# Optimization experiments

Measured on AMD Instinct MI355X. Metric: run time of the kernel, lower is better.

## Reference

```python
import jax, jax.numpy as jnp
import numpy as np
from jax import lax

B, C, IC, H, W = 4, 64, 32, 64, 64


def _conv(x, w, b, stride, pad):
    y = lax.conv_general_dilated(
        x, w, (stride, stride), [(pad, pad), (pad, pad)],
        dimension_numbers=('NCHW', 'OIHW', 'NCHW'))
    return y + b[None, :, None, None]


def setup_inputs() -> dict:
    key = jax.random.key(0)
    ks = jax.random.split(key, 15)
    s = 0.05
    inp = {
        'x': jax.random.normal(ks[0], (B, C, H, W), jnp.float32),
        # GEunit convs (3x3)
        'd1_w': jax.random.normal(ks[1], (C, C, 3, 3), jnp.float32) * s,
        'd1_b': jax.random.normal(ks[2], (C,), jnp.float32) * s,
        'd2_w': jax.random.normal(ks[3], (C, C, 3, 3), jnp.float32) * s,
        'd2_b': jax.random.normal(ks[4], (C,), jnp.float32) * s,
        'd3_w': jax.random.normal(ks[5], (C, C, 3, 3), jnp.float32) * s,
        'd3_b': jax.random.normal(ks[6], (C,), jnp.float32) * s,
        # 1x1 projections
        'g_w': jax.random.normal(ks[7], (IC, C, 1, 1), jnp.float32) * s,
        'g_b': jax.random.normal(ks[8], (IC,), jnp.float32) * s,
        'th_w': jax.random.normal(ks[9], (IC, C, 1, 1), jnp.float32) * s,
        'th_b': jax.random.normal(ks[10], (IC,), jnp.float32) * s,
        'ph_w': jax.random.normal(ks[11], (IC, C, 1, 1), jnp.float32) * s,
        'ph_b': jax.random.normal(ks[12], (IC,), jnp.float32) * s,
        # output projection (zero-init in original; random here for nontrivial baseline)
        'w_w': jax.random.normal(ks[13], (C, IC, 1, 1), jnp.float32) * s,
        'w_b': jax.random.normal(ks[14], (C,), jnp.float32) * s,
    }
    return inp


def _forward(x, d1_w, d1_b, d2_w, d2_b, d3_w, d3_b,
             g_w, g_b, th_w, th_b, ph_w, ph_b, w_w, w_b):
    lrelu = lambda v: jnp.where(v >= 0, v, 0.2 * v)
    y = lrelu(_conv(x, d1_w, d1_b, 2, 1))
    y = lrelu(_conv(y, d2_w, d2_b, 2, 1))
    y = _conv(y, d3_w, d3_b, 2, 1)
    y = jax.image.resize(y, (x.shape[0], x.shape[1], x.shape[2], x.shape[3]),
                         method='bilinear')  # align_corners=False equivalent
    am = jax.nn.sigmoid(y) * x  # attention_map, [B,C,H,W]

    b, c, h, w = am.shape
    n = h * w
    g_x = _conv(am, g_w, g_b, 1, 0).reshape(b, IC, n)      # [B,IC,N]
    theta = _conv(am, th_w, th_b, 1, 0).reshape(b, IC, n)  # [B,IC,N]
    phi = _conv(am, ph_w, ph_b, 1, 0).reshape(b, IC, n)    # [B,IC,N]

    # f[b,i,j] = theta[:, i] . phi[:, j];  softmax over dim=1 (the i axis)
    f = jnp.einsum('bci,bcj->bij', theta, phi)             # [B,N,N]
    f_div_C = jax.nn.softmax(f, axis=1)
    y2 = jnp.einsum('bij,bjc->bic', f_div_C, g_x.transpose(0, 2, 1))  # [B,N,IC]
    y2 = y2.transpose(0, 2, 1).reshape(b, IC, h, w)

    W_y = _conv(y2, w_w, w_b, 1, 0)
    z = W_y + am
    return z * x


def reference(x, d1_w, d1_b, d2_w, d2_b, d3_w, d3_b,
              g_w, g_b, th_w, th_b, ph_w, ph_b, w_w, w_b):
    return _forward(x, d1_w, d1_b, d2_w, d2_b, d3_w, d3_b,
                    g_w, g_b, th_w, th_b, ph_w, ph_b, w_w, w_b)
```

## Files before the change

### kernel.cpp

```cpp
#include <hip/hip_runtime.h>

#define B_ 4
#define C_ 64
#define IC_ 32
#define N_ 4096
#define LOG2E 1.44269504088896341f

typedef __attribute__((ext_vector_type(8))) short short8;
typedef __attribute__((ext_vector_type(4))) float floatx4;
typedef unsigned short ushort_t;

__device__ __forceinline__ unsigned short f2bf(float f) {
  unsigned u = __float_as_uint(f);
  u += 0x7FFFu + ((u >> 16) & 1u);
  return (unsigned short)(u >> 16);
}
__device__ __forceinline__ float bf2f(unsigned short h) {
  return __uint_as_float(((unsigned)h) << 16);
}

__global__ void __launch_bounds__(256) pack_xw_k(
    const float* __restrict__ x, unsigned short* __restrict__ xclp,
    const float* __restrict__ d1_w, const float* __restrict__ d2_w, const float* __restrict__ d3_w,
    const float* __restrict__ th_w, const float* __restrict__ ph_w, const float* __restrict__ g_w,
    const float* __restrict__ th_b, const float* __restrict__ ph_b, const float* __restrict__ g_b,
    unsigned short* __restrict__ wpk, unsigned short* __restrict__ wproj, float* __restrict__ bproj)
{
  __shared__ float s[64][65];
  const int t = threadIdx.x;
  if (blockIdx.x < 256) {
    const int b = blockIdx.x >> 6, h = blockIdx.x & 63;
    for (int idx = t; idx < 4096; idx += 256) {
      int c = idx >> 6, w = idx & 63;
      s[c][w] = x[((size_t)(b * 64 + c)) * 4096 + h * 64 + w];
    }
    __syncthreads();
    for (int idx = t; idx < 4096; idx += 256) {
      int w = idx >> 6, c = idx & 63;
      xclp[(((size_t)b * 66 + h + 1) * 66 + (w + 1)) * 64 + c] = f2bf(s[c][w]);
    }
  } else {
    const int tid = (blockIdx.x - 256) * 256 + t;
    for (int idx = tid; idx < 3 * 36864; idx += 16 * 256) {
      int cv = idx / 36864, r = idx % 36864;
      int tap = r / 4096, r2 = r % 4096;
      int oc = r2 >> 6, ic = r2 & 63;
      const float* src = (cv == 0) ? d1_w : (cv == 1) ? d2_w : d3_w;
      wpk[(size_t)cv * 36864 + tap * 4096 + oc * 64 + ic] = f2bf(src[oc * 576 + ic * 9 + tap]);
    }
    for (int idx = tid; idx < 6144; idx += 16 * 256) {
      int m = idx >> 6, ic = idx & 63;
      float v = (m < 32) ? LOG2E * th_w[m * 64 + ic]
              : (m < 64) ? ph_w[(m - 32) * 64 + ic]
                         : g_w[(m - 64) * 64 + ic];
      wproj[m * 64 + ic] = f2bf(v);
    }
    for (int m = tid; m < 96; m += 16 * 256) {
      bproj[m] = (m < 32) ? LOG2E * th_b[m] : (m < 64) ? ph_b[m - 32] : g_b[m - 64];
    }
  }
}

template<int IN_PW, int OUT_H, bool LRELU, bool OUT_BF16>
__global__ void __launch_bounds__(64) convmf_k(
    const unsigned short* __restrict__ xin, const unsigned short* __restrict__ wp,
    const float* __restrict__ bias, unsigned short* __restrict__ obf,
    float* __restrict__ of32)
{
  constexpr int NTILES = OUT_H * OUT_H / 16;
  const int lane = threadIdx.x;
  const int n15 = lane & 15, quad = lane >> 4;
  int bx = blockIdx.x;
  const int octile = bx & 3; bx >>= 2;
  const int otile = bx % NTILES;
  const int b = bx / NTILES;
  const int o = otile * 16 + n15;
  const int oh = o / OUT_H, ow = o % OUT_H;
  const unsigned short* xb = xin + (size_t)b * IN_PW * IN_PW * 64;
  floatx4 acc = {0.f, 0.f, 0.f, 0.f};
#pragma unroll
  for (int tap = 0; tap < 9; ++tap) {
    const int kh = tap / 3, kw = tap % 3;
    const unsigned short* xpix = xb + ((size_t)(oh * 2 + kh) * IN_PW + (ow * 2 + kw)) * 64;
#pragma unroll
    for (int ks = 0; ks < 2; ++ks) {
      short8 af = *reinterpret_cast<const short8*>(
          wp + ((size_t)tap * 64 + octile * 16 + n15) * 64 + ks * 32 + quad * 8);
      short8 bf = *reinterpret_cast<const short8*>(xpix + ks * 32 + quad * 8);
      acc = __builtin_amdgcn_mfma_f32_16x16x32_bf16(af, bf, acc, 0, 0, 0);
    }
  }
  const float4 bv = *reinterpret_cast<const float4*>(bias + octile * 16 + quad * 4);
  float v[4] = {acc[0] + bv.x, acc[1] + bv.y, acc[2] + bv.z, acc[3] + bv.w};
  if (LRELU) {
#pragma unroll
    for (int r = 0; r < 4; ++r) v[r] = (v[r] >= 0.f) ? v[r] : 0.2f * v[r];
  }
  if (OUT_BF16) {
    constexpr int OPW = OUT_H + 2;
    unsigned short pk[4];
#pragma unroll
    for (int r = 0; r < 4; ++r) pk[r] = f2bf(v[r]);
    *reinterpret_cast<uint2*>(
        obf + (((size_t)b * OPW + oh + 1) * OPW + (ow + 1)) * 64 + octile * 16 + quad * 4) =
        *reinterpret_cast<uint2*>(pk);
  } else {
    *reinterpret_cast<float4*>(
        of32 + ((size_t)b * OUT_H * OUT_H + o) * 64 + octile * 16 + quad * 4) =
        *reinterpret_cast<float4*>(v);
  }
}

__global__ void __launch_bounds__(256) upsproj_k(
    const unsigned short* __restrict__ y2clp, const unsigned short* __restrict__ wp3,
    const float* __restrict__ b3, const float* __restrict__ x,
    const unsigned short* __restrict__ wproj, const float* __restrict__ bproj,
    unsigned short* __restrict__ am_cl, unsigned short* __restrict__ thph,
    unsigned short* __restrict__ g16)
{
  const int b = blockIdx.x >> 6, oh = blockIdx.x & 63;
  const int t = threadIdx.x;
  __shared__ float s0[512], s1[512];
  __shared__ unsigned short s_am[64][72];
  float sh = (oh + 0.5f) * 0.125f - 0.5f;
  float fh = floorf(sh); float ah = sh - fh; int h0 = (int)fh;
  int h0c = min(7, max(0, h0)), h1c = min(7, max(0, h0 + 1));
  {
    const int wave = t >> 6, lane = t & 63;
    const int n15 = lane & 15, quad = lane >> 4;
    const int hrow = (n15 < 8) ? h0c : h1c;
    const int ow8 = n15 & 7;
    const unsigned short* xb2 = y2clp + (size_t)b * 18 * 18 * 64;
    floatx4 acc = {0.f, 0.f, 0.f, 0.f};
#pragma unroll
    for (int tap = 0; tap < 9; ++tap) {
      const int kh = tap / 3, kw = tap % 3;
      const unsigned short* xpix = xb2 + ((size_t)(hrow * 2 + kh) * 18 + (ow8 * 2 + kw)) * 64;
#pragma unroll
      for (int ks = 0; ks < 2; ++ks) {
        short8 af = *reinterpret_cast<const short8*>(
            wp3 + ((size_t)tap * 64 + wave * 16 + n15) * 64 + ks * 32 + quad * 8);
        short8 bf = *reinterpret_cast<const short8*>(xpix + ks * 32 + quad * 8);
        acc = __builtin_amdgcn_mfma_f32_16x16x32_bf16(af, bf, acc, 0, 0, 0);
      }
    }
    const float4 bv = *reinterpret_cast<const float4*>(b3 + wave * 16 + quad * 4);
    float4 st = {acc[0] + bv.x, acc[1] + bv.y, acc[2] + bv.z, acc[3] + bv.w};
    float* dst = (n15 < 8) ? s0 : s1;
    *reinterpret_cast<float4*>(&dst[(size_t)ow8 * 64 + wave * 16 + quad * 4]) = st;
  }
  __syncthreads();
  {
    const int ow = t >> 2, cq = t & 3;
    float sw = (ow + 0.5f) * 0.125f - 0.5f;
    float fw = floorf(sw); float aw = sw - fw; int w0 = (int)fw;
    int w0c = min(7, max(0, w0)), w1c = min(7, max(0, w0 + 1));
    const int n = oh * 64 + ow;
    const float* xb = x + (size_t)b * 64 * 4096 + n;
    unsigned short* ap = am_cl + ((size_t)b * N_ + n) * 64 + cq * 16;
#pragma unroll
    for (int u = 0; u < 4; ++u) {
      int c0 = cq * 16 + u * 4;
      float4 a00 = *reinterpret_cast<const float4*>(&s0[w0c * 64 + c0]);
      float4 a01 = *reinterpret_cast<const float4*>(&s0[w1c * 64 + c0]);
      float4 a10 = *reinterpret_cast<const float4*>(&s1[w0c * 64 + c0]);
      float4 a11 = *reinterpret_cast<const float4*>(&s1[w1c * 64 + c0]);
      float i0[4] = {a00.x * (1.f - aw) + a01.x * aw, a00.y * (1.f - aw) + a01.y * aw,
                     a00.z * (1.f - aw) + a01.z * aw, a00.w * (1.f - aw) + a01.w * aw};
      float i1[4] = {a10.x * (1.f - aw) + a11.x * aw, a10.y * (1.f - aw) + a11.y * aw,
                     a10.z * (1.f - aw) + a11.z * aw, a10.w * (1.f - aw) + a11.w * aw};
      unsigned short pk[4];
#pragma unroll
      for (int vi = 0; vi < 4; ++vi) {
        float vv = i0[vi] * (1.f - ah) + i1[vi] * ah;
        float xv = xb[(size_t)(c0 + vi) * 4096];
        float sig = 1.f / (1.f + __expf(-vv));
        pk[vi] = f2bf(sig * xv);
      }
      uint2 pkt = *reinterpret_cast<uint2*>(pk);
      *reinterpret_cast<uint2*>(ap + u * 4) = pkt;
      *reinterpret_cast<uint2*>(&s_am[ow][c0]) = pkt;
    }
  }
  __syncthreads();
  const int wave = t >> 6, lane = t & 63;
  const int n15 = lane & 15, quad = lane >> 4;
  const int n = oh * 64 + wave * 16 + n15;
  const unsigned short* srow = &s_am[wave * 16 + n15][0];
  const short8 bf0 = *reinterpret_cast<const short8*>(srow + quad * 8);
  const short8 bf1 = *reinterpret_cast<const short8*>(srow + 32 + quad * 8);
#pragma unroll
  for (int mt = 0; mt < 6; ++mt) {
    short8 a0 = *reinterpret_cast<const short8*>(wproj + ((size_t)mt * 16 + n15) * 64 + quad * 8);
    short8 a1 = *reinterpret_cast<const short8*>(wproj + ((size_t)mt * 16 + n15) * 64 + 32 + quad * 8);
    floatx4 acc = {0.f, 0.f, 0.f, 0.f};
    acc = __builtin_amdgcn_mfma_f32_16x16x32_bf16(a0, bf0, acc, 0, 0, 0);
    acc = __builtin_amdgcn_mfma_f32_16x16x32_bf16(a1, bf1, acc, 0, 0, 0);
    const float4 bv = *reinterpret_cast<const float4*>(bproj + mt * 16 + quad * 4);
    float v[4] = {acc[0] + bv.x, acc[1] + bv.y, acc[2] + bv.z, acc[3] + bv.w};
    if (mt < 4) {
      unsigned short pk[4];
#pragma unroll
      for (int r = 0; r < 4; ++r) pk[r] = f2bf(v[r]);
      *reinterpret_cast<uint2*>(thph + ((size_t)b * N_ + n) * 64 + mt * 16 + quad * 4) =
          *reinterpret_cast<uint2*>(pk);
    } else {
#pragma unroll
      for (int r = 0; r < 4; ++r)
        g16[((size_t)b * 32 + (mt - 4) * 16 + quad * 4 + r) * N_ + n] = f2bf(v[r]);
    }
  }
}

__global__ void __launch_bounds__(256) attn_stats_k(
    const unsigned short* __restrict__ thph, float* __restrict__ lpart)
{
  const int b  = blockIdx.y;
  const int iz = blockIdx.z;
  const int t = threadIdx.x, wave = t >> 6, lane = t & 63;
  const int n15 = lane & 15, quad = lane >> 4;
  const int jw = blockIdx.x * 256 + wave * 64;
  const unsigned short* base = thph + (size_t)b * N_ * 64;
  short8 bv[4];
#pragma unroll
  for (int v = 0; v < 4; ++v)
    bv[v] = *reinterpret_cast<const short8*>(base + (size_t)(jw + v * 16 + n15) * 64 + 32 + quad * 8);
  float ls[4] = {0.f, 0.f, 0.f, 0.f};
  const unsigned short* ap = base + (size_t)(iz * 256 + n15) * 64 + quad * 8;
  short8 ac = *reinterpret_cast<const short8*>(ap);
  for (int st = 0; st < 16; ++st) {
    short8 an = *reinterpret_cast<const short8*>(ap + (size_t)((st < 15) ? st + 1 : st) * 1024);
#pragma unroll
    for (int v = 0; v < 4; ++v) {
      floatx4 z = {0.f, 0.f, 0.f, 0.f};
      z = __builtin_amdgcn_mfma_f32_16x16x32_bf16(ac, bv[v], z, 0, 0, 0);
      ls[v] += (__builtin_amdgcn_exp2f(z[0]) + __builtin_amdgcn_exp2f(z[1]))
             + (__builtin_amdgcn_exp2f(z[2]) + __builtin_amdgcn_exp2f(z[3]));
    }
    ac = an;
  }
#pragma unroll
  for (int v = 0; v < 4; ++v) {
    ls[v] += __shfl_xor(ls[v], 16);
    ls[v] += __shfl_xor(ls[v], 32);
  }
  if (quad == 0) {
#pragma unroll
    for (int v = 0; v < 4; ++v)
      lpart[((size_t)iz * B_ + b) * N_ + jw + v * 16 + n15] = ls[v];
  }
}

__global__ void __launch_bounds__(256) scale_g_k(
    const float* __restrict__ lpart, unsigned short* __restrict__ g16)
{
  const int b = blockIdx.y;
  const int c0 = blockIdx.z * 8;
  const int j = blockIdx.x * 256 + threadIdx.x;
  float l = 0.f;
#pragma unroll
  for (int iz = 0; iz < 16; ++iz) l += lpart[((size_t)iz * B_ + b) * N_ + j];
  const float rl = 1.f / l;
  unsigned short* gp = g16 + ((size_t)b * 32 + c0) * N_ + j;
#pragma unroll
  for (int c = 0; c < 8; ++c) {
    gp[(size_t)c * N_] = f2bf(bf2f(gp[(size_t)c * N_]) * rl);
  }
}

#define PHI_PITCH 40
#define G_PITCH   136
__global__ void __launch_bounds__(256, 2) attn_pv_k(
    const unsigned short* __restrict__ thph, const unsigned short* __restrict__ g16,
    unsigned short* __restrict__ y2p)
{
  const int b  = blockIdx.y;
  const int jq = blockIdx.z;
  const int t = threadIdx.x, wave = t >> 6, lane = t & 63;
  const int n15 = lane & 15, quad = lane >> 4;
  const int iw = blockIdx.x * 128 + wave * 32;
  const unsigned short* base = thph + (size_t)b * N_ * 64;
  const unsigned short* gs   = g16  + (size_t)b * 32 * N_;
  __shared__ unsigned short phi_lds[2][128 * PHI_PITCH];
  __shared__ unsigned short g_lds[2][32 * G_PITCH];

  const short8 bth0 = *reinterpret_cast<const short8*>(base + (size_t)(iw + n15) * 64 + quad * 8);
  const short8 bth1 = *reinterpret_cast<const short8*>(base + (size_t)(iw + 16 + n15) * 64 + quad * 8);
  floatx4 Y00 = {0.f, 0.f, 0.f, 0.f}, Y01 = {0.f, 0.f, 0.f, 0.f};
  floatx4 Y10 = {0.f, 0.f, 0.f, 0.f}, Y11 = {0.f, 0.f, 0.f, 0.f};

  const int rphi = wave * 32 + (lane >> 2), cph = lane & 3;
  const int cg   = wave * 8  + (lane >> 4), chg = lane & 15;

  uint4 sp0, sp1, sg0, sg1;
  const int jbase = jq * 1024;
  sp0 = *reinterpret_cast<const uint4*>(base + (size_t)(jbase + rphi) * 64 + 32 + cph * 8);
  sp1 = *reinterpret_cast<const uint4*>(base + (size_t)(jbase + rphi + 16) * 64 + 32 + cph * 8);
  sg0 = *reinterpret_cast<const uint4*>(gs + (size_t)cg * N_ + jbase + chg * 8);
  sg1 = *reinterpret_cast<const uint4*>(gs + (size_t)(cg + 4) * N_ + jbase + chg * 8);
  *reinterpret_cast<uint4*>(&phi_lds[0][rphi * PHI_PITCH + cph * 8]) = sp0;
  *reinterpret_cast<uint4*>(&phi_lds[0][(rphi + 16) * PHI_PITCH + cph * 8]) = sp1;
  *reinterpret_cast<uint4*>(&g_lds[0][cg * G_PITCH + chg * 8]) = sg0;
  *reinterpret_cast<uint4*>(&g_lds[0][(cg + 4) * G_PITCH + chg * 8]) = sg1;
  __syncthreads();

  int j0 = jbase;
  for (int ch = 0; ch < 8; ++ch, j0 += 128) {
    const int cur = ch & 1;
    if (ch < 7) {
      const int jn = j0 + 128;
      sp0 = *reinterpret_cast<const uint4*>(base + (size_t)(jn + rphi) * 64 + 32 + cph * 8);
      sp1 = *reinterpret_cast<const uint4*>(base + (size_t)(jn + rphi + 16) * 64 + 32 + cph * 8);
      sg0 = *reinterpret_cast<const uint4*>(gs + (size_t)cg * N_ + jn + chg * 8);
      sg1 = *reinterpret_cast<const uint4*>(gs + (size_t)(cg + 4) * N_ + jn + chg * 8);
    }
    const unsigned short* phb = &phi_lds[cur][0];
    const unsigned short* glb = &g_lds[cur][0];
#pragma unroll
    for (int sg = 0; sg < 4; ++sg) {
      unsigned pk0[4], pk1[4];
#pragma unroll
      for (int jtl = 0; jtl < 2; ++jtl) {
        const int jt = sg * 2 + jtl;
        short8 aph = *reinterpret_cast<const short8*>(phb + (jt * 16 + n15) * PHI_PITCH + quad * 8);
        floatx4 z0 = {0.f, 0.f, 0.f, 0.f}, z1 = {0.f, 0.f, 0.f, 0.f};
        z0 = __builtin_amdgcn_mfma_f32_16x16x32_bf16(aph, bth0, z0, 0, 0, 0);
        z1 = __builtin_amdgcn_mfma_f32_16x16x32_bf16(aph, bth1, z1, 0, 0, 0);
        float a0 = __builtin_amdgcn_exp2f(z0[0]), a1 = __builtin_amdgcn_exp2f(z0[1]);
        float a2 = __builtin_amdgcn_exp2f(z0[2]), a3 = __builtin_amdgcn_exp2f(z0[3]);
        float b0f = __builtin_amdgcn_exp2f(z1[0]), b1f = __builtin_amdgcn_exp2f(z1[1]);
        float b2f = __builtin_amdgcn_exp2f(z1[2]), b3f = __builtin_amdgcn_exp2f(z1[3]);
        pk0[jtl * 2 + 0] = __builtin_amdgcn_perm(__float_as_uint(a1), __float_as_uint(a0), 0x07060302);
        pk0[jtl * 2 + 1] = __builtin_amdgcn_perm(__float_as_uint(a3), __float_as_uint(a2), 0x07060302);
        pk1[jtl * 2 + 0] = __builtin_amdgcn_perm(__float_as_uint(b1f), __float_as_uint(b0f), 0x07060302);
        pk1[jtl * 2 + 1] = __builtin_amdgcn_perm(__float_as_uint(b3f), __float_as_uint(b2f), 0x07060302);
      }
      union { unsigned u[4]; short8 v; } pa0, pa1, gb0, gb1;
      pa0.u[0] = pk0[0]; pa0.u[1] = pk0[1]; pa0.u[2] = pk0[2]; pa0.u[3] = pk0[3];
      pa1.u[0] = pk1[0]; pa1.u[1] = pk1[1]; pa1.u[2] = pk1[2]; pa1.u[3] = pk1[3];
      const unsigned short* gr0 = glb + n15 * G_PITCH + sg * 32 + quad * 4;
      const unsigned short* gr1 = glb + (16 + n15) * G_PITCH + sg * 32 + quad * 4;
      uint2 lo0 = *reinterpret_cast<const uint2*>(gr0);
      uint2 hi0 = *reinterpret_cast<const uint2*>(gr0 + 16);
      uint2 lo1 = *reinterpret_cast<const uint2*>(gr1);
      uint2 hi1 = *reinterpret_cast<const uint2*>(gr1 + 16);
      gb0.u[0] = lo0.x; gb0.u[1] = lo0.y; gb0.u[2] = hi0.x; gb0.u[3] = hi0.y;
      gb1.u[0] = lo1.x; gb1.u[1] = lo1.y; gb1.u[2] = hi1.x; gb1.u[3] = hi1.y;
      Y00 = __builtin_amdgcn_mfma_f32_16x16x32_bf16(pa0.v, gb0.v, Y00, 0, 0, 0);
      Y01 = __builtin_amdgcn_mfma_f32_16x16x32_bf16(pa0.v, gb1.v, Y01, 0, 0, 0);
      Y10 = __builtin_amdgcn_mfma_f32_16x16x32_bf16(pa1.v, gb0.v, Y10, 0, 0, 0);
      Y11 = __builtin_amdgcn_mfma_f32_16x16x32_bf16(pa1.v, gb1.v, Y11, 0, 0, 0);
    }
    if (ch < 7) {
      const int nb = cur ^ 1;
      *reinterpret_cast<uint4*>(&phi_lds[nb][rphi * PHI_PITCH + cph * 8]) = sp0;
      *reinterpret_cast<uint4*>(&phi_lds[nb][(rphi + 16) * PHI_PITCH + cph * 8]) = sp1;
      *reinterpret_cast<uint4*>(&g_lds[nb][cg * G_PITCH + chg * 8]) = sg0;
      *reinterpret_cast<uint4*>(&g_lds[nb][(cg + 4) * G_PITCH + chg * 8]) = sg1;
    }
    __syncthreads();
  }
  unsigned w00[2], w01[2], w10[2], w11[2];
  w00[0] = ((unsigned)f2bf(Y00[1]) << 16) | f2bf(Y00[0]);
  w00[1] = ((unsigned)f2bf(Y00[3]) << 16) | f2bf(Y00[2]);
  w01[0] = ((unsigned)f2bf(Y01[1]) << 16) | f2bf(Y01[0]);
  w01[1] = ((unsigned)f2bf(Y01[3]) << 16) | f2bf(Y01[2]);
  w10[0] = ((unsigned)f2bf(Y10[1]) << 16) | f2bf(Y10[0]);
  w10[1] = ((unsigned)f2bf(Y10[3]) << 16) | f2bf(Y10[2]);
  w11[0] = ((unsigned)f2bf(Y11[1]) << 16) | f2bf(Y11[0]);
  w11[1] = ((unsigned)f2bf(Y11[3]) << 16) | f2bf(Y11[2]);
  const size_t orow = ((size_t)jq * B_ + b) * 32;
  *reinterpret_cast<uint2*>(y2p + (orow + n15) * N_ + iw + quad * 4) =
      *reinterpret_cast<uint2*>(w00);
  *reinterpret_cast<uint2*>(y2p + (orow + 16 + n15) * N_ + iw + quad * 4) =
      *reinterpret_cast<uint2*>(w01);
  *reinterpret_cast<uint2*>(y2p + (orow + n15) * N_ + iw + 16 + quad * 4) =
      *reinterpret_cast<uint2*>(w10);
  *reinterpret_cast<uint2*>(y2p + (orow + 16 + n15) * N_ + iw + 16 + quad * 4) =
      *reinterpret_cast<uint2*>(w11);
}

__global__ void __launch_bounds__(256) final_k(
    const unsigned short* __restrict__ y2p, const float* __restrict__ w_w,
    const float* __restrict__ w_b, const unsigned short* __restrict__ am_cl,
    const float* __restrict__ x, float* __restrict__ out)
{
  const int n0 = (blockIdx.x * 256 + threadIdx.x) * 2;
  const int o0 = blockIdx.y * 8;
  const int b  = blockIdx.z;
  float a0[8], a1[8];
#pragma unroll
  for (int u = 0; u < 8; ++u) { a0[u] = w_b[o0 + u]; a1[u] = a0[u]; }
  for (int c = 0; c < 32; ++c) {
    float s0 = 0.f, s1 = 0.f;
#pragma unroll
    for (int ph = 0; ph < 4; ++ph) {
      unsigned v = *reinterpret_cast<const unsigned*>(
          y2p + (((size_t)ph * B_ + b) * 32 + c) * N_ + n0);
      s0 += bf2f((unsigned short)(v & 0xffffu));
      s1 += bf2f((unsigned short)(v >> 16));
    }
#pragma unroll
    for (int u = 0; u < 8; ++u) {
      float wv = w_w[(o0 + u) * 32 + c];
      a0[u] += wv * s0; a1[u] += wv * s1;
    }
  }
  const short8 am0 = *reinterpret_cast<const short8*>(am_cl + ((size_t)b * N_ + n0) * 64 + o0);
  const short8 am1 = *reinterpret_cast<const short8*>(am_cl + ((size_t)b * N_ + n0 + 1) * 64 + o0);
#pragma unroll
  for (int u = 0; u < 8; ++u) {
    size_t off = ((size_t)b * 64 + o0 + u) * N_ + n0;
    float2 xv = *reinterpret_cast<const float2*>(x + off);
    float2 ov;
    ov.x = (a0[u] + bf2f((unsigned short)am0[u])) * xv.x;
    ov.y = (a1[u] + bf2f((unsigned short)am1[u])) * xv.y;
    *reinterpret_cast<float2*>(out + off) = ov;
  }
}

extern "C" void kernel_launch(void* const* d_in, const int* in_sizes, int n_in,
                              void* d_out, int out_size, void* d_ws, size_t ws_size,
                              hipStream_t stream) {
  const float* x    = (const float*)d_in[0];
  const float* d1_w = (const float*)d_in[1];
  const float* d1_b = (const float*)d_in[2];
  const float* d2_w = (const float*)d_in[3];
  const float* d2_b = (const float*)d_in[4];
  const float* d3_w = (const float*)d_in[5];
  const float* d3_b = (const float*)d_in[6];
  const float* g_w  = (const float*)d_in[7];
  const float* g_b  = (const float*)d_in[8];
  const float* th_w = (const float*)d_in[9];
  const float* th_b = (const float*)d_in[10];
  const float* ph_w = (const float*)d_in[11];
  const float* ph_b = (const float*)d_in[12];
  const float* w_w  = (const float*)d_in[13];
  const float* w_b  = (const float*)d_in[14];
  float* out = (float*)d_out;

  char* p = (char*)d_ws;
  unsigned short* am_cl = (unsigned short*)p;  p += (size_t)B_ * N_ * 64 * 2;
  unsigned short* thph  = (unsigned short*)p;  p += (size_t)B_ * N_ * 64 * 2;
  unsigned short* g16   = (unsigned short*)p;  p += (size_t)B_ * 32 * N_ * 2;
  float* lpart          = (float*)p;           p += (size_t)16 * B_ * N_ * 4;
  unsigned short* y2p   = (unsigned short*)p;  p += (size_t)4 * B_ * 32 * N_ * 2;
  unsigned short* wpk   = (unsigned short*)p;  p += (size_t)3 * 36864 * 2;
  unsigned short* wproj = (unsigned short*)p;  p += (size_t)96 * 64 * 2;
  float* bproj          = (float*)p;           p += (size_t)96 * 4;
  char* zbase = p;
  unsigned short* xclp  = (unsigned short*)p;  p += (size_t)B_ * 66 * 66 * 64 * 2;
  unsigned short* y1clp = (unsigned short*)p;  p += (size_t)B_ * 34 * 34 * 64 * 2;
  unsigned short* y2clp = (unsigned short*)p;  p += (size_t)B_ * 18 * 18 * 64 * 2;
  const size_t zbytes = (size_t)(p - zbase);

  hipMemsetAsync(zbase, 0, zbytes, stream);
  pack_xw_k<<<272, 256, 0, stream>>>(x, xclp, d1_w, d2_w, d3_w, th_w, ph_w, g_w,
                                     th_b, ph_b, g_b, wpk, wproj, bproj);
  convmf_k<66, 32, true,  true ><<<1024, 64, 0, stream>>>(xclp,  wpk,         d1_b, y1clp, nullptr);
  convmf_k<34, 16, true,  true ><<<256,  64, 0, stream>>>(y1clp, wpk + 36864, d2_b, y2clp, nullptr);
  upsproj_k<<<256, 256, 0, stream>>>(y2clp, wpk + 2 * 36864, d3_b, x, wproj, bproj,
                                     am_cl, thph, g16);
  attn_stats_k<<<dim3(16, 4, 16), 256, 0, stream>>>(thph, lpart);
  scale_g_k<<<dim3(16, 4, 4), 256, 0, stream>>>(lpart, g16);
  attn_pv_k<<<dim3(32, 4, 4), 256, 0, stream>>>(thph, g16, y2p);
  final_k<<<dim3(8, 8, 4), 256, 0, stream>>>(y2p, w_w, w_b, am_cl, x, out);
}
```

Measured before the change: 151.6 us.

## Fuse softmax normalization into PV kernel, drop memset, widen stats tiles

Removes the separate scale_g kernel: attn_pv_k now reduces the column-sum partials into an LDS reciprocal table and scales g while staging it into LDS. Replaces the full workspace memset with border-only zeroing of the padded buffers inside pack_xw_k. attn_stats_k now gives each wave 128 columns instead of 64, halving the grid and reusing each theta load across more MFMAs. This saves two launches and some memory traffic, but each PV block redundantly sums the 16 partials for its columns, and the stats kernel uses more registers with fewer blocks.

```diff
diff --git a/kernel.cpp b/kernel.cpp
--- a/kernel.cpp
+++ b/kernel.cpp
@@ -8,7 +8,6 @@
 
 typedef __attribute__((ext_vector_type(8))) short short8;
 typedef __attribute__((ext_vector_type(4))) float floatx4;
-typedef unsigned short ushort_t;
 
 __device__ __forceinline__ unsigned short f2bf(float f) {
   unsigned u = __float_as_uint(f);
@@ -24,7 +23,8 @@
     const float* __restrict__ d1_w, const float* __restrict__ d2_w, const float* __restrict__ d3_w,
     const float* __restrict__ th_w, const float* __restrict__ ph_w, const float* __restrict__ g_w,
     const float* __restrict__ th_b, const float* __restrict__ ph_b, const float* __restrict__ g_b,
-    unsigned short* __restrict__ wpk, unsigned short* __restrict__ wproj, float* __restrict__ bproj)
+    unsigned short* __restrict__ wpk, unsigned short* __restrict__ wproj, float* __restrict__ bproj,
+    unsigned short* __restrict__ y1clp, unsigned short* __restrict__ y2clp)
 {
   __shared__ float s[64][65];
   const int t = threadIdx.x;
@@ -57,6 +57,31 @@
     }
     for (int m = tid; m < 96; m += 16 * 256) {
       bproj[m] = (m < 32) ? LOG2E * th_b[m] : (m < 64) ? ph_b[m - 32] : g_b[m - 64];
+    }
+    const uint4 z4 = {0u, 0u, 0u, 0u};
+    for (int idx = tid; idx < 4 * 4356; idx += 4096) {
+      int r = idx % 4356, h = r / 66, w = r % 66;
+      if (h == 0 || h == 65 || w == 0 || w == 65) {
+        uint4* d = reinterpret_cast<uint4*>(xclp + (size_t)idx * 64);
+#pragma unroll
+        for (int q = 0; q < 8; ++q) d[q] = z4;
+      }
+    }
+    for (int idx = tid; idx < 4 * 1156; idx += 4096) {
+      int r = idx % 1156, h = r / 34, w = r % 34;
+      if (h == 0 || h == 33 || w == 0 || w == 33) {
+        uint4* d = reinterpret_cast<uint4*>(y1clp + (size_t)idx * 64);
+#pragma unroll
+        for (int q = 0; q < 8; ++q) d[q] = z4;
+      }
+    }
+    for (int idx = tid; idx < 4 * 324; idx += 4096) {
+      int r = idx % 324, h = r / 18, w = r % 18;
+      if (h == 0 || h == 17 || w == 0 || w == 17) {
+        uint4* d = reinterpret_cast<uint4*>(y2clp + (size_t)idx * 64);
+#pragma unroll
+        for (int q = 0; q < 8; ++q) d[q] = z4;
+      }
     }
   }
 }
@@ -219,19 +244,21 @@
   const int iz = blockIdx.z;
   const int t = threadIdx.x, wave = t >> 6, lane = t & 63;
   const int n15 = lane & 15, quad = lane >> 4;
-  const int jw = blockIdx.x * 256 + wave * 64;
+  const int jw = blockIdx.x * 512 + wave * 128;
   const unsigned short* base = thph + (size_t)b * N_ * 64;
-  short8 bv[4];
-#pragma unroll
-  for (int v = 0; v < 4; ++v)
+  short8 bv[8];
+#pragma unroll
+  for (int v = 0; v < 8; ++v)
     bv[v] = *reinterpret_cast<const short8*>(base + (size_t)(jw + v * 16 + n15) * 64 + 32 + quad * 8);
-  float ls[4] = {0.f, 0.f, 0.f, 0.f};
+  float ls[8];
+#pragma unroll
+  for (int v = 0; v < 8; ++v) ls[v] = 0.f;
   const unsigned short* ap = base + (size_t)(iz * 256 + n15) * 64 + quad * 8;
   short8 ac = *reinterpret_cast<const short8*>(ap);
   for (int st = 0; st < 16; ++st) {
     short8 an = *reinterpret_cast<const short8*>(ap + (size_t)((st < 15) ? st + 1 : st) * 1024);
 #pragma unroll
-    for (int v = 0; v < 4; ++v) {
+    for (int v = 0; v < 8; ++v) {
       floatx4 z = {0.f, 0.f, 0.f, 0.f};
       z = __builtin_amdgcn_mfma_f32_16x16x32_bf16(ac, bv[v], z, 0, 0, 0);
       ls[v] += (__builtin_amdgcn_exp2f(z[0]) + __builtin_amdgcn_exp2f(z[1]))
@@ -240,31 +267,14 @@
     ac = an;
   }
 #pragma unroll
-  for (int v = 0; v < 4; ++v) {
+  for (int v = 0; v < 8; ++v) {
     ls[v] += __shfl_xor(ls[v], 16);
     ls[v] += __shfl_xor(ls[v], 32);
   }
   if (quad == 0) {
 #pragma unroll
-    for (int v = 0; v < 4; ++v)
+    for (int v = 0; v < 8; ++v)
       lpart[((size_t)iz * B_ + b) * N_ + jw + v * 16 + n15] = ls[v];
-  }
-}
-
-__global__ void __launch_bounds__(256) scale_g_k(
-    const float* __restrict__ lpart, unsigned short* __restrict__ g16)
-{
-  const int b = blockIdx.y;
-  const int c0 = blockIdx.z * 8;
-  const int j = blockIdx.x * 256 + threadIdx.x;
-  float l = 0.f;
-#pragma unroll
-  for (int iz = 0; iz < 16; ++iz) l += lpart[((size_t)iz * B_ + b) * N_ + j];
-  const float rl = 1.f / l;
-  unsigned short* gp = g16 + ((size_t)b * 32 + c0) * N_ + j;
-#pragma unroll
-  for (int c = 0; c < 8; ++c) {
-    gp[(size_t)c * N_] = f2bf(bf2f(gp[(size_t)c * N_]) * rl);
   }
 }
 
@@ -272,7 +282,7 @@
 #define G_PITCH   136
 __global__ void __launch_bounds__(256, 2) attn_pv_k(
     const unsigned short* __restrict__ thph, const unsigned short* __restrict__ g16,
-    unsigned short* __restrict__ y2p)
+    const float* __restrict__ lpart, unsigned short* __restrict__ y2p)
 {
   const int b  = blockIdx.y;
   const int jq = blockIdx.z;
@@ -283,6 +293,15 @@
   const unsigned short* gs   = g16  + (size_t)b * 32 * N_;
   __shared__ unsigned short phi_lds[2][128 * PHI_PITCH];
   __shared__ unsigned short g_lds[2][32 * G_PITCH];
+  __shared__ float rl_lds[1024];
+
+  const int jbase = jq * 1024;
+  for (int jj = t; jj < 1024; jj += 256) {
+    float l = 0.f;
+#pragma unroll
+    for (int iz = 0; iz < 16; ++iz) l += lpart[((size_t)iz * B_ + b) * N_ + jbase + jj];
+    rl_lds[jj] = 1.f / l;
+  }
 
   const short8 bth0 = *reinterpret_cast<const short8*>(base + (size_t)(iw + n15) * 64 + quad * 8);
   const short8 bth1 = *reinterpret_cast<const short8*>(base + (size_t)(iw + 16 + n15) * 64 + quad * 8);
@@ -293,15 +312,34 @@
   const int cg   = wave * 8  + (lane >> 4), chg = lane & 15;
 
   uint4 sp0, sp1, sg0, sg1;
-  const int jbase = jq * 1024;
   sp0 = *reinterpret_cast<const uint4*>(base + (size_t)(jbase + rphi) * 64 + 32 + cph * 8);
   sp1 = *reinterpret_cast<const uint4*>(base + (size_t)(jbase + rphi + 16) * 64 + 32 + cph * 8);
   sg0 = *reinterpret_cast<const uint4*>(gs + (size_t)cg * N_ + jbase + chg * 8);
   sg1 = *reinterpret_cast<const uint4*>(gs + (size_t)(cg + 4) * N_ + jbase + chg * 8);
-  *reinterpret_cast<uint4*>(&phi_lds[0][rphi * PHI_PITCH + cph * 8]) = sp0;
-  *reinterpret_cast<uint4*>(&phi_lds[0][(rphi + 16) * PHI_PITCH + cph * 8]) = sp1;
-  *reinterpret_cast<uint4*>(&g_lds[0][cg * G_PITCH + chg * 8]) = sg0;
-  *reinterpret_cast<uint4*>(&g_lds[0][(cg + 4) * G_PITCH + chg * 8]) = sg1;
+  __syncthreads();
+
+#define PV_WRITE_STAGE(BUF, CHN)                                                     \
+  {                                                                                  \
+    *reinterpret_cast<uint4*>(&phi_lds[BUF][rphi * PHI_PITCH + cph * 8]) = sp0;      \
+    *reinterpret_cast<uint4*>(&phi_lds[BUF][(rphi + 16) * PHI_PITCH + cph * 8]) = sp1;\
+    const int jloc = (CHN) * 128 + chg * 8;                                          \
+    float4 r0 = *reinterpret_cast<const float4*>(&rl_lds[jloc]);                     \
+    float4 r1 = *reinterpret_cast<const float4*>(&rl_lds[jloc + 4]);                 \
+    union U8s { uint4 u4; unsigned short us[8]; } ua, ub, oa, ob_;                   \
+    ua.u4 = sg0; ub.u4 = sg1;                                                        \
+    oa.us[0] = f2bf(bf2f(ua.us[0]) * r0.x); oa.us[1] = f2bf(bf2f(ua.us[1]) * r0.y);  \
+    oa.us[2] = f2bf(bf2f(ua.us[2]) * r0.z); oa.us[3] = f2bf(bf2f(ua.us[3]) * r0.w);  \
+    oa.us[4] = f2bf(bf2f(ua.us[4]) * r1.x); oa.us[5] = f2bf(bf2f(ua.us[5]) * r1.y);  \
+    oa.us[6] = f2bf(bf2f(ua.us[6]) * r1.z); oa.us[7] = f2bf(bf2f(ua.us[7]) * r1.w);  \
+    ob_.us[0] = f2bf(bf2f(ub.us[0]) * r0.x); ob_.us[1] = f2bf(bf2f(ub.us[1]) * r0.y);\
+    ob_.us[2] = f2bf(bf2f(ub.us[2]) * r0.z); ob_.us[3] = f2bf(bf2f(ub.us[3]) * r0.w);\
+    ob_.us[4] = f2bf(bf2f(ub.us[4]) * r1.x); ob_.us[5] = f2bf(bf2f(ub.us[5]) * r1.y);\
+    ob_.us[6] = f2bf(bf2f(ub.us[6]) * r1.z); ob_.us[7] = f2bf(bf2f(ub.us[7]) * r1.w);\
+    *reinterpret_cast<uint4*>(&g_lds[BUF][cg * G_PITCH + chg * 8]) = oa.u4;          \
+    *reinterpret_cast<uint4*>(&g_lds[BUF][(cg + 4) * G_PITCH + chg * 8]) = ob_.u4;   \
+  }
+
+  PV_WRITE_STAGE(0, 0)
   __syncthreads();
 
   int j0 = jbase;
@@ -353,13 +391,11 @@
     }
     if (ch < 7) {
       const int nb = cur ^ 1;
-      *reinterpret_cast<uint4*>(&phi_lds[nb][rphi * PHI_PITCH + cph * 8]) = sp0;
-      *reinterpret_cast<uint4*>(&phi_lds[nb][(rphi + 16) * PHI_PITCH + cph * 8]) = sp1;
-      *reinterpret_cast<uint4*>(&g_lds[nb][cg * G_PITCH + chg * 8]) = sg0;
-      *reinterpret_cast<uint4*>(&g_lds[nb][(cg + 4) * G_PITCH + chg * 8]) = sg1;
+      PV_WRITE_STAGE(nb, ch + 1)
     }
     __syncthreads();
   }
+#undef PV_WRITE_STAGE
   unsigned w00[2], w01[2], w10[2], w11[2];
   w00[0] = ((unsigned)f2bf(Y00[1]) << 16) | f2bf(Y00[0]);
   w00[1] = ((unsigned)f2bf(Y00[3]) << 16) | f2bf(Y00[2]);
@@ -448,21 +484,17 @@
   unsigned short* wpk   = (unsigned short*)p;  p += (size_t)3 * 36864 * 2;
   unsigned short* wproj = (unsigned short*)p;  p += (size_t)96 * 64 * 2;
   float* bproj          = (float*)p;           p += (size_t)96 * 4;
-  char* zbase = p;
   unsigned short* xclp  = (unsigned short*)p;  p += (size_t)B_ * 66 * 66 * 64 * 2;
   unsigned short* y1clp = (unsigned short*)p;  p += (size_t)B_ * 34 * 34 * 64 * 2;
   unsigned short* y2clp = (unsigned short*)p;  p += (size_t)B_ * 18 * 18 * 64 * 2;
-  const size_t zbytes = (size_t)(p - zbase);
-
-  hipMemsetAsync(zbase, 0, zbytes, stream);
+
   pack_xw_k<<<272, 256, 0, stream>>>(x, xclp, d1_w, d2_w, d3_w, th_w, ph_w, g_w,
-                                     th_b, ph_b, g_b, wpk, wproj, bproj);
+                                     th_b, ph_b, g_b, wpk, wproj, bproj, y1clp, y2clp);
   convmf_k<66, 32, true,  true ><<<1024, 64, 0, stream>>>(xclp,  wpk,         d1_b, y1clp, nullptr);
   convmf_k<34, 16, true,  true ><<<256,  64, 0, stream>>>(y1clp, wpk + 36864, d2_b, y2clp, nullptr);
   upsproj_k<<<256, 256, 0, stream>>>(y2clp, wpk + 2 * 36864, d3_b, x, wproj, bproj,
                                      am_cl, thph, g16);
-  attn_stats_k<<<dim3(16, 4, 16), 256, 0, stream>>>(thph, lpart);
-  scale_g_k<<<dim3(16, 4, 4), 256, 0, stream>>>(lpart, g16);
-  attn_pv_k<<<dim3(32, 4, 4), 256, 0, stream>>>(thph, g16, y2p);
+  attn_stats_k<<<dim3(8, 4, 16), 256, 0, stream>>>(thph, lpart);
+  attn_pv_k<<<dim3(32, 4, 4), 256, 0, stream>>>(thph, g16, lpart, y2p);
   final_k<<<dim3(8, 8, 4), 256, 0, stream>>>(y2p, w_w, w_b, am_cl, x, out);
 }
```

Measured after the change: 152.5 us. No clear change (+0.6%).
